# Kernel optimization log

Hardware: AMD Instinct MI355X
Metric: run time of the kernel (lower is better)

Reference implementation:

```python
import jax, jax.numpy as jnp
import numpy as np

N_HEADS = 16

def setup_inputs() -> dict:
    key = jax.random.key(0)
    k1, k2, k3 = jax.random.split(key, 3)
    d = 1024
    x = jax.random.normal(k1, (4, 2048, d), dtype=jnp.float32)
    w_qkv = jax.random.normal(k2, (d, 3 * d), dtype=jnp.float32) * (1.0 / np.sqrt(d))
    w_proj = jax.random.normal(k3, (d, d), dtype=jnp.float32) * (1.0 / np.sqrt(d))
    return {"x": x, "w_qkv": w_qkv, "w_proj": w_proj}

def reference(x, w_qkv, w_proj):
    b, s, c = x.shape
    h = N_HEADS
    hd = c // h
    qkv = x @ w_qkv  # [b, s, 3c]
    q, k, v = jnp.split(qkv, 3, axis=-1)
    # [b, h, s, hd]
    q = q.reshape(b, s, h, hd).transpose(0, 2, 1, 3)
    k = k.reshape(b, s, h, hd).transpose(0, 2, 1, 3)
    v = v.reshape(b, s, h, hd).transpose(0, 2, 1, 3)
    scores = jnp.einsum('bhqd,bhkd->bhqk', q, k) / jnp.sqrt(jnp.float32(hd))
    causal = jnp.tril(jnp.ones((s, s), dtype=bool))
    scores = jnp.where(causal[None, None], scores, jnp.float32(-jnp.inf))
    attn = jax.nn.softmax(scores, axis=-1)
    out = jnp.einsum('bhqk,bhkd->bhqd', attn, v)
    out = out.transpose(0, 2, 1, 3).reshape(b, s, c)
    return out @ w_proj
```

## Files before the change

kernel.cpp:

```cpp
#include <hip/hip_runtime.h>
#include <hip/hip_bf16.h>

typedef unsigned short u16;
typedef __attribute__((ext_vector_type(8))) short short8;
typedef __attribute__((ext_vector_type(4))) float f32x4;
typedef __attribute__((ext_vector_type(16))) float f32x16;

__device__ inline u16 f2bf(float f) {
  unsigned u = __float_as_uint(f);
  u += 0x7fffu + ((u >> 16) & 1u);
  return (u16)(u >> 16);
}

__global__ __launch_bounds__(256) void cast_kernel(const float* __restrict__ in,
                                                   u16* __restrict__ out, int n4) {
  int i = blockIdx.x * 256 + threadIdx.x;
  if (i >= n4) return;
  float4 v = ((const float4*)in)[i];
  ushort4 o;
  o.x = f2bf(v.x); o.y = f2bf(v.y); o.z = f2bf(v.z); o.w = f2bf(v.w);
  ((ushort4*)out)[i] = o;
}

__global__ __launch_bounds__(256) void tcast_kernel(const float* __restrict__ in,
                                                    u16* __restrict__ out, int K, int N) {
  __shared__ float tile[32][33];
  int bx = blockIdx.x * 32;
  int by = blockIdx.y * 32;
  int tx = threadIdx.x & 31, ty = threadIdx.x >> 5;
#pragma unroll
  for (int i = 0; i < 4; i++) {
    int r = ty + i * 8;
    tile[r][tx] = in[(size_t)(by + r) * N + bx + tx];
  }
  __syncthreads();
#pragma unroll
  for (int i = 0; i < 4; i++) {
    int r = ty + i * 8;
    out[(size_t)(bx + r) * K + by + tx] = f2bf(tile[tx][r]);
  }
}

__global__ __launch_bounds__(256) void pack_kv(const u16* __restrict__ kbuf,
                                               const u16* __restrict__ vbuf,
                                               u16* __restrict__ kpack,
                                               u16* __restrict__ vpack) {
  __shared__ __align__(16) u16 ktile[64 * 72];
  __shared__ __align__(16) u16 vtile[64 * 72];
  int t = threadIdx.x;
  int kt = blockIdx.x, h = blockIdx.y, b = blockIdx.z;
  int bh = b * 16 + h;
  size_t rb = (size_t)(b * 2048 + kt * 64);
#pragma unroll
  for (int i = 0; i < 2; i++) {
    int idx = i * 256 + t; int r = idx >> 3, c8 = (idx & 7) * 8;
    *(uint4*)&ktile[r * 72 + c8] = *(const uint4*)(kbuf + (rb + r) * 1024 + h * 64 + c8);
    *(uint4*)&vtile[r * 72 + c8] = *(const uint4*)(vbuf + (rb + r) * 1024 + h * 64 + c8);
  }
  __syncthreads();
  u16* kd = kpack + ((size_t)bh * 32 + kt) * 4096;
  u16* vd = vpack + ((size_t)bh * 32 + kt) * 4096;
#pragma unroll
  for (int i = 0; i < 2; i++) {
    int idx = i * 256 + t;
    int j = idx >> 6, lane = idx & 63, l31 = lane & 31, hi5 = lane >> 5;
    *(uint4*)(kd + j * 512 + lane * 8) =
        *(const uint4*)&ktile[((j >> 2) * 32 + l31) * 72 + (j & 3) * 16 + hi5 * 8];
    union { u16 s[8]; uint4 u; } pv;
#pragma unroll
    for (int e = 0; e < 8; e++)
      pv.s[e] = vtile[((j & 3) * 16 + hi5 * 8 + e) * 72 + (j >> 2) * 32 + l31];
    *(uint4*)(vd + j * 512 + lane * 8) = pv.u;
  }
}

#define GEMM_BODY(KSTR)                                                                       \
  __shared__ __align__(16) u16 As[128 * 32];                                                  \
  __shared__ __align__(16) u16 Bs[128 * 32];                                                  \
  int t = threadIdx.x;                                                                        \
  int wave = t >> 6, lane = t & 63, l15 = lane & 15, quad = lane >> 4;                        \
  int bn = blockIdx.x * 128, bm = blockIdx.y * 128;                                           \
  int wm = (wave >> 1) * 64, wn = (wave & 1) * 64;                                            \
  f32x4 acc[4][4];                                                                            \
  for (int i = 0; i < 4; i++)                                                                 \
    for (int j = 0; j < 4; j++) acc[i][j] = (f32x4)0.0f;                                      \
  int srow = wave * 16 + (lane >> 2);                                                         \
  int scol = (lane & 3) * 8;                                                                  \
  const u16* ga0 = A + (size_t)(bm + srow) * KSTR + scol;                                     \
  const u16* ga1 = A + (size_t)(bm + 64 + srow) * KSTR + scol;                                \
  const u16* gb0 = Bt + (size_t)(bn + srow) * KSTR + scol;                                    \
  const u16* gb1 = Bt + (size_t)(bn + 64 + srow) * KSTR + scol;                               \
  u16* lA0 = As + wave * 512;                                                                 \
  u16* lA1 = As + 2048 + wave * 512;                                                          \
  u16* lB0 = Bs + wave * 512;                                                                 \
  u16* lB1 = Bs + 2048 + wave * 512;                                                          \
  for (int k0 = 0; k0 < KSTR; k0 += 32) {                                                     \
    __syncthreads();                                                                          \
    __builtin_amdgcn_global_load_lds((const __attribute__((address_space(1))) unsigned*)(ga0 + k0), \
                                     (__attribute__((address_space(3))) unsigned*)lA0, 16, 0, 0);   \
    __builtin_amdgcn_global_load_lds((const __attribute__((address_space(1))) unsigned*)(ga1 + k0), \
                                     (__attribute__((address_space(3))) unsigned*)lA1, 16, 0, 0);   \
    __builtin_amdgcn_global_load_lds((const __attribute__((address_space(1))) unsigned*)(gb0 + k0), \
                                     (__attribute__((address_space(3))) unsigned*)lB0, 16, 0, 0);   \
    __builtin_amdgcn_global_load_lds((const __attribute__((address_space(1))) unsigned*)(gb1 + k0), \
                                     (__attribute__((address_space(3))) unsigned*)lB1, 16, 0, 0);   \
    __syncthreads();                                                                          \
    short8 a[4], b[4];                                                                        \
    for (int mt = 0; mt < 4; mt++)                                                            \
      a[mt] = *(const short8*)(&As[(wm + mt * 16 + l15) * 32 + quad * 8]);                    \
    for (int nt = 0; nt < 4; nt++)                                                            \
      b[nt] = *(const short8*)(&Bs[(wn + nt * 16 + l15) * 32 + quad * 8]);                    \
    for (int mt = 0; mt < 4; mt++)                                                            \
      for (int nt = 0; nt < 4; nt++)                                                          \
        acc[mt][nt] = __builtin_amdgcn_mfma_f32_16x16x32_bf16(a[mt], b[nt], acc[mt][nt], 0, 0, 0); \
  }

__global__ __launch_bounds__(256) void gemm_qkv(const u16* __restrict__ A,
                                                const u16* __restrict__ Bt,
                                                u16* __restrict__ qb,
                                                u16* __restrict__ kb,
                                                u16* __restrict__ vb) {
  GEMM_BODY(1024)
  u16* dst = (bn < 1024) ? qb : (bn < 2048) ? kb : vb;
  float scl = (bn < 1024) ? 0.18033688011112f : 1.0f;
  int bnl = bn & 1023;
#pragma unroll
  for (int mt = 0; mt < 4; mt++)
#pragma unroll
    for (int nt = 0; nt < 4; nt++)
#pragma unroll
      for (int r = 0; r < 4; r++) {
        int row = bm + wm + mt * 16 + quad * 4 + r;
        int col = bnl + wn + nt * 16 + l15;
        dst[(size_t)row * 1024 + col] = f2bf(acc[mt][nt][r] * scl);
      }
}

__global__ __launch_bounds__(256) void gemm_proj(const u16* __restrict__ A,
                                                 const u16* __restrict__ Bt,
                                                 float* __restrict__ Co) {
  GEMM_BODY(1024)
#pragma unroll
  for (int mt = 0; mt < 4; mt++)
#pragma unroll
    for (int nt = 0; nt < 4; nt++)
#pragma unroll
      for (int r = 0; r < 4; r++) {
        int row = bm + wm + mt * 16 + quad * 4 + r;
        int col = bn + wn + nt * 16 + l15;
        Co[(size_t)row * 1024 + col] = acc[mt][nt][r];
      }
}

__global__ __launch_bounds__(256, 2) void attn_kernel(const u16* __restrict__ qbuf,
                                                      const u16* __restrict__ kpack,
                                                      const u16* __restrict__ vpack,
                                                      u16* __restrict__ ctx) {
  int t = threadIdx.x;
  int wave = t >> 6, lane = t & 63, l31 = lane & 31, hi = lane >> 5;
  int bh = blockIdx.x;
  int s = (int)blockIdx.y * 4 + wave;
  int b = bh >> 4, h = bh & 15;
  int rowbase = b * 2048;
  int hi4 = hi * 4;

  const u16* kp = kpack + (size_t)bh * (32 * 4096) + lane * 8;
  const u16* vp = vpack + (size_t)bh * (32 * 4096) + lane * 8;

#pragma unroll
  for (int ph = 0; ph < 2; ph++) {
    int strip = ph ? 63 - s : s;
    int q0 = strip * 32;
    int q_lane = q0 + l31;

    const u16* qp = qbuf + (size_t)(rowbase + q_lane) * 1024 + h * 64 + hi * 8;
    short8 qf[4];
#pragma unroll
    for (int ks = 0; ks < 4; ks++) qf[ks] = *(const short8*)(qp + ks * 16);

    float l_run = 0.0f;
    f32x16 o[2];
    o[0] = (f32x16)0.0f; o[1] = (f32x16)0.0f;
    int ktmax = (q0 + 31) >> 6;

    for (int kt = 0; kt <= ktmax; kt++) {
      const u16* kb = kp + kt * 4096;
      const u16* vb = vp + kt * 4096;

      short8 ka[8], vv[8];
#pragma unroll
      for (int j = 0; j < 8; j++) {
        ka[j] = *(const short8*)(kb + j * 512);
        vv[j] = *(const short8*)(vb + j * 512);
      }

      f32x16 st0 = (f32x16)0.0f, st1 = (f32x16)0.0f;
#pragma unroll
      for (int ks = 0; ks < 4; ks++) {
        st0 = __builtin_amdgcn_mfma_f32_32x32x16_bf16(ka[ks], qf[ks], st0, 0, 0, 0);
        st1 = __builtin_amdgcn_mfma_f32_32x32x16_bf16(ka[4 + ks], qf[ks], st1, 0, 0, 0);
      }

      unsigned pk[2][8];
      if (kt == ktmax) {
#pragma unroll
        for (int ii = 0; ii < 8; ii++) {
          int key = kt * 64 + ((2 * ii) & 3) + 8 * ((2 * ii) >> 2) + hi4;
          float p00 = (key     <= q_lane) ? __builtin_amdgcn_exp2f(st0[2 * ii])     : 0.0f;
          float p01 = (key + 1 <= q_lane) ? __builtin_amdgcn_exp2f(st0[2 * ii + 1]) : 0.0f;
          float p10 = (key + 32 <= q_lane) ? __builtin_amdgcn_exp2f(st1[2 * ii])     : 0.0f;
          float p11 = (key + 33 <= q_lane) ? __builtin_amdgcn_exp2f(st1[2 * ii + 1]) : 0.0f;
          l_run += p00 + p01 + p10 + p11;
          pk[0][ii] = ((__float_as_uint(p00) + 0x8000u) >> 16) |
                      ((__float_as_uint(p01) + 0x8000u) & 0xffff0000u);
          pk[1][ii] = ((__float_as_uint(p10) + 0x8000u) >> 16) |
                      ((__float_as_uint(p11) + 0x8000u) & 0xffff0000u);
        }
      } else {
#pragma unroll
        for (int ii = 0; ii < 8; ii++) {
          float p00 = __builtin_amdgcn_exp2f(st0[2 * ii]);
          float p01 = __builtin_amdgcn_exp2f(st0[2 * ii + 1]);
          float p10 = __builtin_amdgcn_exp2f(st1[2 * ii]);
          float p11 = __builtin_amdgcn_exp2f(st1[2 * ii + 1]);
          l_run += p00 + p01 + p10 + p11;
          pk[0][ii] = ((__float_as_uint(p00) + 0x8000u) >> 16) |
                      ((__float_as_uint(p01) + 0x8000u) & 0xffff0000u);
          pk[1][ii] = ((__float_as_uint(p10) + 0x8000u) >> 16) |
                      ((__float_as_uint(p11) + 0x8000u) & 0xffff0000u);
        }
      }

      short8 pf[4];
#pragma unroll
      for (int ks2 = 0; ks2 < 4; ks2++) {
        int km = ks2 >> 1, h4 = (ks2 & 1) * 4;
        unsigned A0 = pk[km][h4 + 0], A1 = pk[km][h4 + 1];
        unsigned B0 = pk[km][h4 + 2], B1 = pk[km][h4 + 3];
        unsigned tA0 = (unsigned)__shfl_xor((int)A0, 32);
        unsigned tA1 = (unsigned)__shfl_xor((int)A1, 32);
        unsigned tB0 = (unsigned)__shfl_xor((int)B0, 32);
        unsigned tB1 = (unsigned)__shfl_xor((int)B1, 32);
        union { unsigned u[4]; short8 sh; } fr;
        fr.u[0] = hi ? tB0 : A0;
        fr.u[1] = hi ? tB1 : A1;
        fr.u[2] = hi ? B0 : tA0;
        fr.u[3] = hi ? B1 : tA1;
        pf[ks2] = fr.sh;
      }

#pragma unroll
      for (int am = 0; am < 2; am++)
#pragma unroll
        for (int ks2 = 0; ks2 < 4; ks2++)
          o[am] = __builtin_amdgcn_mfma_f32_32x32x16_bf16(vv[am * 4 + ks2], pf[ks2], o[am], 0, 0, 0);
    }

    float l_tot = l_run + __shfl_xor(l_run, 32);
    float inv = 1.0f / l_tot;
    size_t obase = (size_t)(rowbase + q_lane) * 1024 + h * 64;
#pragma unroll
    for (int am = 0; am < 2; am++)
#pragma unroll
      for (int k = 0; k < 4; k++) {
        ushort4 w;
        w.x = f2bf(o[am][4 * k + 0] * inv);
        w.y = f2bf(o[am][4 * k + 1] * inv);
        w.z = f2bf(o[am][4 * k + 2] * inv);
        w.w = f2bf(o[am][4 * k + 3] * inv);
        *(ushort4*)&ctx[obase + am * 32 + k * 8 + hi4] = w;
      }
  }
}

extern "C" void kernel_launch(void* const* d_in, const int* in_sizes, int n_in,
                              void* d_out, int out_size, void* d_ws, size_t ws_size,
                              hipStream_t stream) {
  const float* x      = (const float*)d_in[0];
  const float* w_qkv  = (const float*)d_in[1];
  const float* w_proj = (const float*)d_in[2];
  float* out = (float*)d_out;

  char* ws = (char*)d_ws;
  const size_t MB = 1024 * 1024;
  u16* qbuf   = (u16*)(ws);
  u16* kbuf   = (u16*)(ws + 16 * MB);
  u16* vbuf   = (u16*)(ws + 32 * MB);
  u16* xb     = (u16*)(ws + 48 * MB);
  u16* kpack  = (u16*)(ws + 48 * MB);
  u16* vpack  = (u16*)(ws + 64 * MB);
  u16* wqkvT  = (u16*)(ws + 80 * MB);
  u16* wprojT = (u16*)(ws + 86 * MB);
  u16* ctx    = kbuf;

  cast_kernel<<<8192, 256, 0, stream>>>(x, xb, 2097152);
  tcast_kernel<<<dim3(96, 32), 256, 0, stream>>>(w_qkv, wqkvT, 1024, 3072);
  tcast_kernel<<<dim3(32, 32), 256, 0, stream>>>(w_proj, wprojT, 1024, 1024);

  gemm_qkv<<<dim3(24, 64), 256, 0, stream>>>(xb, wqkvT, qbuf, kbuf, vbuf);
  pack_kv<<<dim3(32, 16, 4), 256, 0, stream>>>(kbuf, vbuf, kpack, vpack);
  attn_kernel<<<dim3(64, 8), 256, 0, stream>>>(qbuf, kpack, vpack, ctx);
  gemm_proj<<<dim3(8, 64), 256, 0, stream>>>(ctx, wprojT, out);
}
```

Before: 256.2 us.

## Fuse K/V packing into QKV GEMM epilogue and merge weight transpose-casts

The QKV GEMM epilogue now stages K and V tiles through enlarged shared memory, lays them out in the MFMA-friendly packed format, and writes the packed pages directly. This removes the separate pack_kv kernel and the round trip through unpacked K/V buffers. The two weight transpose-cast launches are merged into one launch. In exchange the GEMM uses 32KB of LDS, which may reduce occupancy, and its epilogue gains extra barriers.

New measurement: 291.0 us. 13.6% more time.

```diff
diff --git a/kernel.cpp b/kernel.cpp
--- a/kernel.cpp
+++ b/kernel.cpp
@@ -22,10 +22,16 @@
   ((ushort4*)out)[i] = o;
 }
 
-__global__ __launch_bounds__(256) void tcast_kernel(const float* __restrict__ in,
-                                                    u16* __restrict__ out, int K, int N) {
+__global__ __launch_bounds__(256) void tcast2_kernel(const float* __restrict__ wqkv,
+                                                     const float* __restrict__ wproj,
+                                                     u16* __restrict__ oqkv,
+                                                     u16* __restrict__ oproj) {
   __shared__ float tile[32][33];
-  int bx = blockIdx.x * 32;
+  int bxr = (int)blockIdx.x;
+  const float* in = (bxr < 96) ? wqkv : wproj;
+  u16* out = (bxr < 96) ? oqkv : oproj;
+  int N = (bxr < 96) ? 3072 : 1024;
+  int bx = ((bxr < 96) ? bxr : bxr - 96) * 32;
   int by = blockIdx.y * 32;
   int tx = threadIdx.x & 31, ty = threadIdx.x >> 5;
 #pragma unroll
@@ -37,109 +43,185 @@
 #pragma unroll
   for (int i = 0; i < 4; i++) {
     int r = ty + i * 8;
-    out[(size_t)(bx + r) * K + by + tx] = f2bf(tile[tx][r]);
-  }
-}
-
-__global__ __launch_bounds__(256) void pack_kv(const u16* __restrict__ kbuf,
-                                               const u16* __restrict__ vbuf,
-                                               u16* __restrict__ kpack,
-                                               u16* __restrict__ vpack) {
-  __shared__ __align__(16) u16 ktile[64 * 72];
-  __shared__ __align__(16) u16 vtile[64 * 72];
+    out[(size_t)(bx + r) * 1024 + by + tx] = f2bf(tile[tx][r]);
+  }
+}
+
+__global__ __launch_bounds__(256) void gemm_qkv_fused(const u16* __restrict__ A,
+                                                      const u16* __restrict__ Bt,
+                                                      u16* __restrict__ qbuf,
+                                                      u16* __restrict__ kpack,
+                                                      u16* __restrict__ vpack) {
+  __shared__ __align__(16) u16 S[16384];
+  u16* As = S;
+  u16* Bs = S + 4096;
   int t = threadIdx.x;
-  int kt = blockIdx.x, h = blockIdx.y, b = blockIdx.z;
-  int bh = b * 16 + h;
-  size_t rb = (size_t)(b * 2048 + kt * 64);
-#pragma unroll
-  for (int i = 0; i < 2; i++) {
-    int idx = i * 256 + t; int r = idx >> 3, c8 = (idx & 7) * 8;
-    *(uint4*)&ktile[r * 72 + c8] = *(const uint4*)(kbuf + (rb + r) * 1024 + h * 64 + c8);
-    *(uint4*)&vtile[r * 72 + c8] = *(const uint4*)(vbuf + (rb + r) * 1024 + h * 64 + c8);
-  }
-  __syncthreads();
-  u16* kd = kpack + ((size_t)bh * 32 + kt) * 4096;
-  u16* vd = vpack + ((size_t)bh * 32 + kt) * 4096;
-#pragma unroll
-  for (int i = 0; i < 2; i++) {
-    int idx = i * 256 + t;
-    int j = idx >> 6, lane = idx & 63, l31 = lane & 31, hi5 = lane >> 5;
-    *(uint4*)(kd + j * 512 + lane * 8) =
-        *(const uint4*)&ktile[((j >> 2) * 32 + l31) * 72 + (j & 3) * 16 + hi5 * 8];
-    union { u16 s[8]; uint4 u; } pv;
-#pragma unroll
-    for (int e = 0; e < 8; e++)
-      pv.s[e] = vtile[((j & 3) * 16 + hi5 * 8 + e) * 72 + (j >> 2) * 32 + l31];
-    *(uint4*)(vd + j * 512 + lane * 8) = pv.u;
-  }
-}
-
-#define GEMM_BODY(KSTR)                                                                       \
-  __shared__ __align__(16) u16 As[128 * 32];                                                  \
-  __shared__ __align__(16) u16 Bs[128 * 32];                                                  \
-  int t = threadIdx.x;                                                                        \
-  int wave = t >> 6, lane = t & 63, l15 = lane & 15, quad = lane >> 4;                        \
-  int bn = blockIdx.x * 128, bm = blockIdx.y * 128;                                           \
-  int wm = (wave >> 1) * 64, wn = (wave & 1) * 64;                                            \
-  f32x4 acc[4][4];                                                                            \
-  for (int i = 0; i < 4; i++)                                                                 \
-    for (int j = 0; j < 4; j++) acc[i][j] = (f32x4)0.0f;                                      \
-  int srow = wave * 16 + (lane >> 2);                                                         \
-  int scol = (lane & 3) * 8;                                                                  \
-  const u16* ga0 = A + (size_t)(bm + srow) * KSTR + scol;                                     \
-  const u16* ga1 = A + (size_t)(bm + 64 + srow) * KSTR + scol;                                \
-  const u16* gb0 = Bt + (size_t)(bn + srow) * KSTR + scol;                                    \
-  const u16* gb1 = Bt + (size_t)(bn + 64 + srow) * KSTR + scol;                               \
-  u16* lA0 = As + wave * 512;                                                                 \
-  u16* lA1 = As + 2048 + wave * 512;                                                          \
-  u16* lB0 = Bs + wave * 512;                                                                 \
-  u16* lB1 = Bs + 2048 + wave * 512;                                                          \
-  for (int k0 = 0; k0 < KSTR; k0 += 32) {                                                     \
-    __syncthreads();                                                                          \
-    __builtin_amdgcn_global_load_lds((const __attribute__((address_space(1))) unsigned*)(ga0 + k0), \
-                                     (__attribute__((address_space(3))) unsigned*)lA0, 16, 0, 0);   \
-    __builtin_amdgcn_global_load_lds((const __attribute__((address_space(1))) unsigned*)(ga1 + k0), \
-                                     (__attribute__((address_space(3))) unsigned*)lA1, 16, 0, 0);   \
-    __builtin_amdgcn_global_load_lds((const __attribute__((address_space(1))) unsigned*)(gb0 + k0), \
-                                     (__attribute__((address_space(3))) unsigned*)lB0, 16, 0, 0);   \
-    __builtin_amdgcn_global_load_lds((const __attribute__((address_space(1))) unsigned*)(gb1 + k0), \
-                                     (__attribute__((address_space(3))) unsigned*)lB1, 16, 0, 0);   \
-    __syncthreads();                                                                          \
-    short8 a[4], b[4];                                                                        \
-    for (int mt = 0; mt < 4; mt++)                                                            \
-      a[mt] = *(const short8*)(&As[(wm + mt * 16 + l15) * 32 + quad * 8]);                    \
-    for (int nt = 0; nt < 4; nt++)                                                            \
-      b[nt] = *(const short8*)(&Bs[(wn + nt * 16 + l15) * 32 + quad * 8]);                    \
-    for (int mt = 0; mt < 4; mt++)                                                            \
-      for (int nt = 0; nt < 4; nt++)                                                          \
-        acc[mt][nt] = __builtin_amdgcn_mfma_f32_16x16x32_bf16(a[mt], b[nt], acc[mt][nt], 0, 0, 0); \
-  }
-
-__global__ __launch_bounds__(256) void gemm_qkv(const u16* __restrict__ A,
-                                                const u16* __restrict__ Bt,
-                                                u16* __restrict__ qb,
-                                                u16* __restrict__ kb,
-                                                u16* __restrict__ vb) {
-  GEMM_BODY(1024)
-  u16* dst = (bn < 1024) ? qb : (bn < 2048) ? kb : vb;
-  float scl = (bn < 1024) ? 0.18033688011112f : 1.0f;
-  int bnl = bn & 1023;
-#pragma unroll
-  for (int mt = 0; mt < 4; mt++)
+  int wave = t >> 6, lane = t & 63, l15 = lane & 15, quad = lane >> 4;
+  int bn = blockIdx.x * 128, bm = blockIdx.y * 128;
+  int wm = (wave >> 1) * 64, wn = (wave & 1) * 64;
+
+  f32x4 acc[4][4];
+#pragma unroll
+  for (int i = 0; i < 4; i++)
+#pragma unroll
+    for (int j = 0; j < 4; j++) acc[i][j] = (f32x4)0.0f;
+
+  int srow = wave * 16 + (lane >> 2);
+  int scol = (lane & 3) * 8;
+  const u16* ga0 = A + (size_t)(bm + srow) * 1024 + scol;
+  const u16* ga1 = A + (size_t)(bm + 64 + srow) * 1024 + scol;
+  const u16* gb0 = Bt + (size_t)(bn + srow) * 1024 + scol;
+  const u16* gb1 = Bt + (size_t)(bn + 64 + srow) * 1024 + scol;
+  u16* lA0 = As + wave * 512;
+  u16* lA1 = As + 2048 + wave * 512;
+  u16* lB0 = Bs + wave * 512;
+  u16* lB1 = Bs + 2048 + wave * 512;
+
+  for (int k0 = 0; k0 < 1024; k0 += 32) {
+    __syncthreads();
+    __builtin_amdgcn_global_load_lds((const __attribute__((address_space(1))) unsigned*)(ga0 + k0),
+                                     (__attribute__((address_space(3))) unsigned*)lA0, 16, 0, 0);
+    __builtin_amdgcn_global_load_lds((const __attribute__((address_space(1))) unsigned*)(ga1 + k0),
+                                     (__attribute__((address_space(3))) unsigned*)lA1, 16, 0, 0);
+    __builtin_amdgcn_global_load_lds((const __attribute__((address_space(1))) unsigned*)(gb0 + k0),
+                                     (__attribute__((address_space(3))) unsigned*)lB0, 16, 0, 0);
+    __builtin_amdgcn_global_load_lds((const __attribute__((address_space(1))) unsigned*)(gb1 + k0),
+                                     (__attribute__((address_space(3))) unsigned*)lB1, 16, 0, 0);
+    __syncthreads();
+
+    short8 a[4], b[4];
+#pragma unroll
+    for (int mt = 0; mt < 4; mt++)
+      a[mt] = *(const short8*)(&As[(wm + mt * 16 + l15) * 32 + quad * 8]);
 #pragma unroll
     for (int nt = 0; nt < 4; nt++)
-#pragma unroll
-      for (int r = 0; r < 4; r++) {
-        int row = bm + wm + mt * 16 + quad * 4 + r;
-        int col = bnl + wn + nt * 16 + l15;
-        dst[(size_t)row * 1024 + col] = f2bf(acc[mt][nt][r] * scl);
-      }
+      b[nt] = *(const short8*)(&Bs[(wn + nt * 16 + l15) * 32 + quad * 8]);
+#pragma unroll
+    for (int mt = 0; mt < 4; mt++)
+#pragma unroll
+      for (int nt = 0; nt < 4; nt++)
+        acc[mt][nt] = __builtin_amdgcn_mfma_f32_16x16x32_bf16(a[mt], b[nt], acc[mt][nt], 0, 0, 0);
+  }
+
+  if (bn < 1024) {
+    const float SCL = 0.18033688011112f;
+#pragma unroll
+    for (int mt = 0; mt < 4; mt++)
+#pragma unroll
+      for (int nt = 0; nt < 4; nt++)
+#pragma unroll
+        for (int r = 0; r < 4; r++) {
+          int row = bm + wm + mt * 16 + quad * 4 + r;
+          int col = bn + wn + nt * 16 + l15;
+          qbuf[(size_t)row * 1024 + col] = f2bf(acc[mt][nt][r] * SCL);
+        }
+  } else {
+    bool isK = bn < 2048;
+    u16* dst = isK ? kpack : vpack;
+    int col0 = bn & 1023;
+    int b = bm >> 11, kt0 = (bm & 2047) >> 6, h0 = col0 >> 6;
+
+    __syncthreads();
+    if (isK) {
+#pragma unroll
+      for (int mt = 0; mt < 4; mt++)
+#pragma unroll
+        for (int nt = 0; nt < 4; nt++)
+#pragma unroll
+          for (int r = 0; r < 4; r++) {
+            int row = wm + mt * 16 + quad * 4 + r;
+            int col = wn + nt * 16 + l15;
+            int key = row & 63, ktl = row >> 6;
+            int hd = col & 63, hl = col >> 6;
+            int off = (4 * (key >> 5) + (hd >> 4)) * 512 + (key & 31) * 8 +
+                      ((hd >> 3) & 1) * 256 + (hd & 7);
+            S[(hl * 2 + ktl) * 4096 + off] = f2bf(acc[mt][nt][r]);
+          }
+    } else {
+#pragma unroll
+      for (int mt = 0; mt < 4; mt++)
+#pragma unroll
+        for (int nt = 0; nt < 4; nt++) {
+          int rowb = wm + mt * 16 + quad * 4;
+          int col = wn + nt * 16 + l15;
+          int keyb = rowb & 63, ktl = rowb >> 6;
+          int hd = col & 63, hl = col >> 6;
+          int off = (4 * (hd >> 5) + (keyb >> 4)) * 512 + (hd & 31) * 8 +
+                    ((keyb >> 3) & 1) * 256 + (keyb & 7);
+          ushort4 w;
+          w.x = f2bf(acc[mt][nt][0]);
+          w.y = f2bf(acc[mt][nt][1]);
+          w.z = f2bf(acc[mt][nt][2]);
+          w.w = f2bf(acc[mt][nt][3]);
+          *(ushort4*)&S[(hl * 2 + ktl) * 4096 + off] = w;
+        }
+    }
+    __syncthreads();
+#pragma unroll
+    for (int c = 0; c < 8; c++) {
+      int lin = c * 256 + t;
+      int page = lin >> 9;
+      int hl = page >> 1, ktl = page & 1;
+      size_t pbase = ((size_t)(b * 16 + h0 + hl) * 32 + (kt0 + ktl)) * 4096;
+      int off = (lin & 511) * 8;
+      *(uint4*)(dst + pbase + off) = *(const uint4*)&S[page * 4096 + off];
+    }
+  }
 }
 
 __global__ __launch_bounds__(256) void gemm_proj(const u16* __restrict__ A,
                                                  const u16* __restrict__ Bt,
                                                  float* __restrict__ Co) {
-  GEMM_BODY(1024)
+  __shared__ __align__(16) u16 As[128 * 32];
+  __shared__ __align__(16) u16 Bs[128 * 32];
+  int t = threadIdx.x;
+  int wave = t >> 6, lane = t & 63, l15 = lane & 15, quad = lane >> 4;
+  int bn = blockIdx.x * 128, bm = blockIdx.y * 128;
+  int wm = (wave >> 1) * 64, wn = (wave & 1) * 64;
+
+  f32x4 acc[4][4];
+#pragma unroll
+  for (int i = 0; i < 4; i++)
+#pragma unroll
+    for (int j = 0; j < 4; j++) acc[i][j] = (f32x4)0.0f;
+
+  int srow = wave * 16 + (lane >> 2);
+  int scol = (lane & 3) * 8;
+  const u16* ga0 = A + (size_t)(bm + srow) * 1024 + scol;
+  const u16* ga1 = A + (size_t)(bm + 64 + srow) * 1024 + scol;
+  const u16* gb0 = Bt + (size_t)(bn + srow) * 1024 + scol;
+  const u16* gb1 = Bt + (size_t)(bn + 64 + srow) * 1024 + scol;
+  u16* lA0 = As + wave * 512;
+  u16* lA1 = As + 2048 + wave * 512;
+  u16* lB0 = Bs + wave * 512;
+  u16* lB1 = Bs + 2048 + wave * 512;
+
+  for (int k0 = 0; k0 < 1024; k0 += 32) {
+    __syncthreads();
+    __builtin_amdgcn_global_load_lds((const __attribute__((address_space(1))) unsigned*)(ga0 + k0),
+                                     (__attribute__((address_space(3))) unsigned*)lA0, 16, 0, 0);
+    __builtin_amdgcn_global_load_lds((const __attribute__((address_space(1))) unsigned*)(ga1 + k0),
+                                     (__attribute__((address_space(3))) unsigned*)lA1, 16, 0, 0);
+    __builtin_amdgcn_global_load_lds((const __attribute__((address_space(1))) unsigned*)(gb0 + k0),
+                                     (__attribute__((address_space(3))) unsigned*)lB0, 16, 0, 0);
+    __builtin_amdgcn_global_load_lds((const __attribute__((address_space(1))) unsigned*)(gb1 + k0),
+                                     (__attribute__((address_space(3))) unsigned*)lB1, 16, 0, 0);
+    __syncthreads();
+
+    short8 a[4], b[4];
+#pragma unroll
+    for (int mt = 0; mt < 4; mt++)
+      a[mt] = *(const short8*)(&As[(wm + mt * 16 + l15) * 32 + quad * 8]);
+#pragma unroll
+    for (int nt = 0; nt < 4; nt++)
+      b[nt] = *(const short8*)(&Bs[(wn + nt * 16 + l15) * 32 + quad * 8]);
+#pragma unroll
+    for (int mt = 0; mt < 4; mt++)
+#pragma unroll
+      for (int nt = 0; nt < 4; nt++)
+        acc[mt][nt] = __builtin_amdgcn_mfma_f32_16x16x32_bf16(a[mt], b[nt], acc[mt][nt], 0, 0, 0);
+  }
+
 #pragma unroll
   for (int mt = 0; mt < 4; mt++)
 #pragma unroll
@@ -206,9 +288,9 @@
 #pragma unroll
         for (int ii = 0; ii < 8; ii++) {
           int key = kt * 64 + ((2 * ii) & 3) + 8 * ((2 * ii) >> 2) + hi4;
-          float p00 = (key     <= q_lane) ? __builtin_amdgcn_exp2f(st0[2 * ii])     : 0.0f;
+          float p00 = (key <= q_lane) ? __builtin_amdgcn_exp2f(st0[2 * ii]) : 0.0f;
           float p01 = (key + 1 <= q_lane) ? __builtin_amdgcn_exp2f(st0[2 * ii + 1]) : 0.0f;
-          float p10 = (key + 32 <= q_lane) ? __builtin_amdgcn_exp2f(st1[2 * ii])     : 0.0f;
+          float p10 = (key + 32 <= q_lane) ? __builtin_amdgcn_exp2f(st1[2 * ii]) : 0.0f;
           float p11 = (key + 33 <= q_lane) ? __builtin_amdgcn_exp2f(st1[2 * ii + 1]) : 0.0f;
           l_run += p00 + p01 + p10 + p11;
           pk[0][ii] = ((__float_as_uint(p00) + 0x8000u) >> 16) |
@@ -284,21 +366,16 @@
   char* ws = (char*)d_ws;
   const size_t MB = 1024 * 1024;
   u16* qbuf   = (u16*)(ws);
-  u16* kbuf   = (u16*)(ws + 16 * MB);
-  u16* vbuf   = (u16*)(ws + 32 * MB);
+  u16* kpack  = (u16*)(ws + 16 * MB);
+  u16* vpack  = (u16*)(ws + 32 * MB);
   u16* xb     = (u16*)(ws + 48 * MB);
-  u16* kpack  = (u16*)(ws + 48 * MB);
-  u16* vpack  = (u16*)(ws + 64 * MB);
-  u16* wqkvT  = (u16*)(ws + 80 * MB);
-  u16* wprojT = (u16*)(ws + 86 * MB);
-  u16* ctx    = kbuf;
+  u16* wqkvT  = (u16*)(ws + 64 * MB);
+  u16* wprojT = (u16*)(ws + 70 * MB);
+  u16* ctx    = xb;
 
   cast_kernel<<<8192, 256, 0, stream>>>(x, xb, 2097152);
-  tcast_kernel<<<dim3(96, 32), 256, 0, stream>>>(w_qkv, wqkvT, 1024, 3072);
-  tcast_kernel<<<dim3(32, 32), 256, 0, stream>>>(w_proj, wprojT, 1024, 1024);
-
-  gemm_qkv<<<dim3(24, 64), 256, 0, stream>>>(xb, wqkvT, qbuf, kbuf, vbuf);
-  pack_kv<<<dim3(32, 16, 4), 256, 0, stream>>>(kbuf, vbuf, kpack, vpack);
+  tcast2_kernel<<<dim3(128, 32), 256, 0, stream>>>(w_qkv, w_proj, wqkvT, wprojT);
+  gemm_qkv_fused<<<dim3(24, 64), 256, 0, stream>>>(xb, wqkvT, qbuf, kpack, vpack);
   attn_kernel<<<dim3(64, 8), 256, 0, stream>>>(qbuf, kpack, vpack, ctx);
   gemm_proj<<<dim3(8, 64), 256, 0, stream>>>(ctx, wprojT, out);
 }
```
